# Kernel tuning notes

Hardware: AMD Instinct MI355X
Metric: run time of the kernel (lower is better)

Reference implementation:

```python
import jax, jax.numpy as jnp
import numpy as np
import math

H = 8
D_MODEL = 512
D_K = D_MODEL // H
DIM_G = 64
WAVE_LEN = 1000.0


def box_relational_embedding(f_g):
    # f_g: [B, N, 4] -> [B, N, N, 64] trigonometric geometry embedding
    x_min, y_min, x_max, y_max = jnp.split(f_g, 4, axis=-1)  # each [B,N,1]
    cx = (x_min + x_max) * 0.5
    cy = (y_min + y_max) * 0.5
    w = x_max - x_min + 1.0
    h = y_max - y_min + 1.0
    # pairwise deltas: [B,N,1] vs [B,1,N] -> [B,N,N]
    cx_t = jnp.swapaxes(cx, 1, 2)  # [B,1,N]
    cy_t = jnp.swapaxes(cy, 1, 2)
    w_t = jnp.swapaxes(w, 1, 2)
    h_t = jnp.swapaxes(h, 1, 2)
    delta_x = jnp.log(jnp.maximum(jnp.abs((cx - cx_t) / w), 0.001))
    delta_y = jnp.log(jnp.maximum(jnp.abs((cy - cy_t) / h), 0.001))
    delta_w = jnp.log(w / w_t)
    delta_h = jnp.log(h / h_t)
    position_mat = jnp.stack([delta_x, delta_y, delta_w, delta_h], axis=-1)  # [B,N,N,4]
    feat_range = jnp.arange(DIM_G // 8, dtype=position_mat.dtype) / (DIM_G / 8)
    dim_mat = 1.0 / jnp.power(jnp.asarray(WAVE_LEN, position_mat.dtype), feat_range)  # [8]
    mul_mat = (100.0 * position_mat)[..., None] * dim_mat  # [B,N,N,4,8]
    B, N = position_mat.shape[0], position_mat.shape[1]
    mul_mat = mul_mat.reshape(B, N, N, -1)  # [B,N,N,32]
    return jnp.concatenate([jnp.sin(mul_mat), jnp.cos(mul_mat)], axis=-1)  # [B,N,N,64]


def setup_inputs() -> dict:
    key = jax.random.key(0)
    ks = jax.random.split(key, 16)
    B, N = 16, 256
    scale = 1.0 / math.sqrt(D_MODEL)
    inp = {
        'input_query': jax.random.normal(ks[0], (B, N, D_MODEL), jnp.float32),
        'input_key': jax.random.normal(ks[1], (B, N, D_MODEL), jnp.float32),
        'input_value': jax.random.normal(ks[2], (B, N, D_MODEL), jnp.float32),
        'input_box': jax.random.uniform(ks[3], (B, N, 4), jnp.float32),
        'mask': jnp.ones((B, N), jnp.int32),
        # projection weights stored as [d_in, d_out] (x @ W + b)
        'Wq': jax.random.normal(ks[4], (D_MODEL, D_MODEL), jnp.float32) * scale,
        'bq': jnp.zeros((D_MODEL,), jnp.float32),
        'Wk': jax.random.normal(ks[5], (D_MODEL, D_MODEL), jnp.float32) * scale,
        'bk': jnp.zeros((D_MODEL,), jnp.float32),
        'Wv': jax.random.normal(ks[6], (D_MODEL, D_MODEL), jnp.float32) * scale,
        'bv': jnp.zeros((D_MODEL,), jnp.float32),
        'Wo': jax.random.normal(ks[7], (D_MODEL, D_MODEL), jnp.float32) * scale,
        'bo': jnp.zeros((D_MODEL,), jnp.float32),
        # 8 geometric-bias heads: Linear(64 -> 1) each, stacked -> [H, 64], [H]
        'WG_w': jax.random.normal(ks[8], (H, DIM_G), jnp.float32) * (1.0 / math.sqrt(DIM_G)),
        'WG_b': jnp.zeros((H,), jnp.float32),
    }
    return inp


def reference(input_query, input_key, input_value, input_box, mask,
              Wq, bq, Wk, bk, Wv, bv, Wo, bo, WG_w, WG_b):
    B, N, _ = input_query.shape

    def proj(x, W, b):  # [B,N,D] -> [B,H,N,d_k]
        return (x @ W + b).reshape(B, N, H, D_K).transpose(0, 2, 1, 3)

    q = proj(input_query, Wq, bq)
    k = proj(input_key, Wk, bk)
    v = proj(input_value, Wv, bv)

    geo = box_relational_embedding(input_box)  # [B,N,N,64]
    # per-head geometric weights, ReLU'd: [B,H,N,N]
    w_g = jax.nn.relu(jnp.einsum('bnmg,hg->bhnm', geo, WG_w) + WG_b[None, :, None, None])

    scaled_dot = jnp.einsum('bhqd,bhkd->bhqk', q, k) / np.sqrt(D_K).astype(q.dtype)
    # mask: [B,N] keys -> [B,1,1,N], broadcast over heads and queries
    scaled_dot = jnp.where(mask[:, None, None, :] == 0, jnp.asarray(-1e9, scaled_dot.dtype), scaled_dot)
    w_mn = jax.nn.softmax(jnp.log(jnp.maximum(w_g, 1e-6)) + scaled_dot, axis=-1)
    # dropout is identity in eval mode
    out = jnp.einsum('bhqk,bhkd->bhqd', w_mn, v)  # [B,H,N,d_k]
    out = out.transpose(0, 2, 1, 3).reshape(B, N, H * D_K)
    return out @ Wo + bo
```

## Files before the change

kernel.cpp:

```cpp
#include <hip/hip_runtime.h>
#include <hip/hip_fp16.h>
#include <math.h>

#define Bv   16
#define Nv   256
#define Dv   512
#define Hv   8
#define MNv  4096

typedef __attribute__((ext_vector_type(8))) short bf16x8;
typedef __attribute__((ext_vector_type(4))) float f32x4;
typedef __fp16 fp16x8 __attribute__((ext_vector_type(8)));
typedef __fp16 fp16x2 __attribute__((ext_vector_type(2)));

__device__ __forceinline__ unsigned short f2bf(float f) {
    unsigned u = __float_as_uint(f);
    u = u + 0x7FFFu + ((u >> 16) & 1u);
    return (unsigned short)(u >> 16);
}
__device__ __forceinline__ void gload_lds16(const void* g, void* l) {
    __builtin_amdgcn_global_load_lds(
        (const __attribute__((address_space(1))) unsigned int*)g,
        (__attribute__((address_space(3))) unsigned int*)l, 16, 0, 0);
}

__device__ __forceinline__ void fast_sincos(float x, float* s, float* c) {
    const float rev = x * 0.15915494309189535f;
    const float fr  = rev - floorf(rev);
    *s = __builtin_amdgcn_sinf(fr);
    *c = __builtin_amdgcn_cosf(fr);
}
__device__ __forceinline__ float fast_log(float x) {
    return __builtin_amdgcn_logf(x) * 0.6931471805599453f;
}
__device__ __forceinline__ float fast_exp(float x) {
    return __builtin_amdgcn_exp2f(x * 1.4426950408889634f);
}

__global__ __launch_bounds__(256) void mega1_kernel(
    const float* __restrict__ box, const int* __restrict__ mask,
    const float* __restrict__ WGw, const float* __restrict__ WGb,
    __half* __restrict__ LB,
    const float* __restrict__ xq, const float* __restrict__ xk,
    const float* __restrict__ xv, unsigned short* __restrict__ Ab,
    const float* __restrict__ Wq, const float* __restrict__ Wk,
    const float* __restrict__ Wv, const float* __restrict__ Wo,
    const float* __restrict__ bq, const float* __restrict__ bk,
    const float* __restrict__ bv, const float* __restrict__ bo,
    unsigned short* __restrict__ Wt, float* __restrict__ biasStack)
{
    __shared__ __align__(16) char smraw[64 * 65 * 4];
    const int bid = blockIdx.x;
    const int t = threadIdx.x;

    if (bid < 4096) {
        unsigned short (*Lst)[264] = (unsigned short (*)[264])smraw;
        const int q = bid & 255;
        const int b = bid >> 8;
        const int w = t >> 6, lane = t & 63;
        const int n = lane & 15;
        const int quad = lane >> 4;

        const float4 bq_ = *(const float4*)(box + (b * Nv + q) * 4);
        const float cxq = (bq_.x + bq_.z) * 0.5f;
        const float cyq = (bq_.y + bq_.w) * 0.5f;
        const float wq  = bq_.z - bq_.x + 1.0f;
        const float hq  = bq_.w - bq_.y + 1.0f;

        union F16x8 { fp16x8 v; fp16x2 p[4]; };
        F16x8 Bs_, Bc_;
        Bs_.v = (fp16x8){}; Bc_.v = (fp16x8){};
        float bias_n = 0.0f;
        if (n < Hv) {
            bias_n = WGb[n];
#pragma unroll
            for (int jj = 0; jj < 4; ++jj) {
                Bs_.p[jj] = __builtin_amdgcn_cvt_pkrtz(WGw[n * 64 + quad * 8 + 2 * jj],
                                                       WGw[n * 64 + quad * 8 + 2 * jj + 1]);
                Bc_.p[jj] = __builtin_amdgcn_cvt_pkrtz(WGw[n * 64 + 32 + quad * 8 + 2 * jj],
                                                       WGw[n * 64 + 32 + quad * 8 + 2 * jj + 1]);
            }
        }

        const float dimm[8] = {1.0f, 0.42169650342f, 0.17782794100f, 0.07498942093f,
                               0.03162277660f, 0.01333521432f, 0.00562341325f, 0.00237137371f};
        const bool isCtr = (quad < 2);
        const bool isY   = (quad & 1);
        const float cq  = isY ? cyq : cxq;
        const float sq_ = isY ? hq : wq;

#pragma unroll
        for (int i = 0; i < 4; ++i) {
            const int m0 = (w * 4 + i) * 16;
            const float4 bm = *(const float4*)(box + (b * Nv + m0 + n) * 4);
            const float cxm = (bm.x + bm.z) * 0.5f;
            const float cym = (bm.y + bm.w) * 0.5f;
            const float wm  = bm.z - bm.x + 1.0f;
            const float hm  = bm.w - bm.y + 1.0f;
            const float cm_ = isY ? cym : cxm;
            const float sm_ = isY ? hm : wm;
            const float top = isCtr ? fabsf(cq - cm_) : sq_;
            const float bot = isCtr ? sq_ : sm_;
            float r = top * __builtin_amdgcn_rcpf(bot);
            if (isCtr) r = fmaxf(r, 1e-3f);
            const float base = 69.31471805599453f * __builtin_amdgcn_logf(r);

            float sv[8], cv[8];
#pragma unroll
            for (int j = 0; j < 8; ++j)
                fast_sincos(base * dimm[j], &sv[j], &cv[j]);

            F16x8 As_, Ac_;
#pragma unroll
            for (int jj = 0; jj < 4; ++jj) {
                As_.p[jj] = __builtin_amdgcn_cvt_pkrtz(sv[2 * jj], sv[2 * jj + 1]);
                Ac_.p[jj] = __builtin_amdgcn_cvt_pkrtz(cv[2 * jj], cv[2 * jj + 1]);
            }

            f32x4 acc = {};
            acc = __builtin_amdgcn_mfma_f32_16x16x32_f16(As_.v, Bs_.v, acc, 0, 0, 0);
            acc = __builtin_amdgcn_mfma_f32_16x16x32_f16(Ac_.v, Bc_.v, acc, 0, 0, 0);

            const int mrow = m0 + quad * 4;
            const int4 mk = *(const int4*)(mask + b * Nv + mrow);
            if (n < Hv) {
                const int* mkp = (const int*)&mk;
                const int pos0 = quad * 64 + (w * 4 + i);
#pragma unroll
                for (int rr = 0; rr < 4; ++rr) {
                    const float val = fmaxf(acc[rr] + bias_n, 1e-6f);
                    const float lb = fast_log(val) + (mkp[rr] ? 0.0f : -30000.0f);
                    Lst[n][pos0 + rr * 16] = __half_as_ushort(__float2half(lb));
                }
            }
        }

        __syncthreads();
        const int h = t >> 5, c = t & 31;
        unsigned short* dst = (unsigned short*)LB +
                              ((size_t)(b * Hv + h) * Nv + q) * Nv + c * 8;
        *(int4*)dst = *(const int4*)&Lst[h][c * 8];

    } else if (bid < 10240) {
        const int i = bid - 4096;
        const int z = i >> 11;
        const int xblk = i & 2047;
        const float* src = (z == 0) ? xq : (z == 1) ? xk : xv;
        const size_t base = (size_t)z * (MNv * Dv);
        const int idx = (xblk * 256 + t) * 4;
        float4 x = *(const float4*)(src + idx);
        ushort4 h4;
        h4.x = f2bf(x.x); h4.y = f2bf(x.y); h4.z = f2bf(x.z); h4.w = f2bf(x.w);
        *(ushort4*)(Ab + base + idx) = h4;

    } else {
        float (*T)[65] = (float (*)[65])smraw;
        const int i = bid - 10240;
        const int z = i >> 6;
        const int rem = i & 63;
        const int n0 = (rem & 7) * 64, k0 = (rem >> 3) * 64;
        const float* W = (z == 0) ? Wq : (z == 1) ? Wk : (z == 2) ? Wv : Wo;
        const float* b = (z == 0) ? bq : (z == 1) ? bk : (z == 2) ? bv : bo;
        const int col = t & 63, rb = t >> 6;
#pragma unroll
        for (int j = 0; j < 16; ++j) {
            const int row = j * 4 + rb;
            T[row][col] = W[(k0 + row) * Dv + n0 + col];
        }
        __syncthreads();
#pragma unroll
        for (int j = 0; j < 16; ++j) {
            const int row = j * 4 + rb;
            Wt[z * (Dv * Dv) + (n0 + row) * Dv + k0 + col] = f2bf(T[col][row]);
        }
        if (rem == 0) {
            biasStack[z * Dv + t]       = b[t];
            biasStack[z * Dv + t + 256] = b[t + 256];
        }
    }
}

__global__ __launch_bounds__(256) void qkv_gemm_kernel(
    const unsigned short* __restrict__ Ab, const unsigned short* __restrict__ Wt,
    const float* __restrict__ bst, unsigned short* __restrict__ Qb2,
    unsigned short* __restrict__ Kb2, unsigned short* __restrict__ Vt2)
{
    const int z = blockIdx.z;
    const unsigned short* A = Ab + (size_t)z * (MNv * Dv);
    const unsigned short* Wz = Wt + (size_t)z * (Dv * Dv);
    const float* bias = bst + z * Dv;

    const int n0 = blockIdx.x * 64;
    const int m0 = blockIdx.y * 128;
    const int t = threadIdx.x;
    const int w = t >> 6, lane = t & 63;
    const int wm = w & 1, wn = w >> 1;

    __shared__ unsigned short As[128][32];
    __shared__ unsigned short Bs[64][32];

    f32x4 acc[4][2] = {};

    const int sr = lane >> 2;
    const int sk = (lane & 3) * 8;
    const int fr = lane & 15;
    const int fk = (lane >> 4) * 8;

    for (int k0 = 0; k0 < Dv; k0 += 32) {
        __syncthreads();
#pragma unroll
        for (int j = 0; j < 2; ++j) {
            const int row = w * 32 + j * 16 + sr;
            gload_lds16(A + (size_t)(m0 + row) * Dv + k0 + sk, &As[w * 32 + j * 16][0]);
        }
        gload_lds16(Wz + (size_t)(n0 + w * 16 + sr) * Dv + k0 + sk, &Bs[w * 16][0]);
        __syncthreads();

        bf16x8 af[4], bfr[2];
#pragma unroll
        for (int mt = 0; mt < 4; ++mt)
            af[mt] = *(const bf16x8*)&As[wm * 64 + mt * 16 + fr][fk];
#pragma unroll
        for (int nt = 0; nt < 2; ++nt)
            bfr[nt] = *(const bf16x8*)&Bs[wn * 32 + nt * 16 + fr][fk];
#pragma unroll
        for (int mt = 0; mt < 4; ++mt)
#pragma unroll
            for (int nt = 0; nt < 2; ++nt)
                acc[mt][nt] = __builtin_amdgcn_mfma_f32_16x16x32_bf16(
                    af[mt], bfr[nt], acc[mt][nt], 0, 0, 0);
    }

    const int er = (lane >> 4) * 4;
    const int ec = lane & 15;
    const float scale = (z == 0) ? 0.125f : 1.0f;
#pragma unroll
    for (int nt = 0; nt < 2; ++nt) {
        const int gn = n0 + wn * 32 + nt * 16 + ec;
        const float bv_ = bias[gn];
#pragma unroll
        for (int mt = 0; mt < 4; ++mt) {
            const int gm = m0 + wm * 64 + mt * 16 + er;
            if (z == 2) {
                ushort4 o;
                o.x = f2bf(acc[mt][nt][0] + bv_);
                o.y = f2bf(acc[mt][nt][1] + bv_);
                o.z = f2bf(acc[mt][nt][2] + bv_);
                o.w = f2bf(acc[mt][nt][3] + bv_);
                *(ushort4*)(Vt2 + ((size_t)(gm >> 8) * Dv + gn) * Nv + (gm & 255)) = o;
            } else {
                unsigned short* cp = ((z == 0) ? Qb2 : Kb2) + (size_t)gm * Dv + gn;
#pragma unroll
                for (int r = 0; r < 4; ++r)
                    cp[(size_t)r * Dv] = f2bf((acc[mt][nt][r] + bv_) * scale);
            }
        }
    }
}

__global__ __launch_bounds__(256) void out_gemm_kernel(
    const unsigned short* __restrict__ A, const unsigned short* __restrict__ Wz,
    const float* __restrict__ bias, float* __restrict__ C)
{
    const int n0 = blockIdx.x * 64;
    const int m0 = blockIdx.y * 128;
    const int t = threadIdx.x;
    const int w = t >> 6, lane = t & 63;
    const int wm = w & 1, wn = w >> 1;

    __shared__ unsigned short As[128][32];
    __shared__ unsigned short Bs[64][32];

    f32x4 acc[4][2] = {};

    const int sr = lane >> 2;
    const int sk = (lane & 3) * 8;
    const int fr = lane & 15;
    const int fk = (lane >> 4) * 8;

    for (int k0 = 0; k0 < Dv; k0 += 32) {
        __syncthreads();
#pragma unroll
        for (int j = 0; j < 2; ++j) {
            const int row = w * 32 + j * 16 + sr;
            gload_lds16(A + (size_t)(m0 + row) * Dv + k0 + sk, &As[w * 32 + j * 16][0]);
        }
        gload_lds16(Wz + (size_t)(n0 + w * 16 + sr) * Dv + k0 + sk, &Bs[w * 16][0]);
        __syncthreads();

        bf16x8 af[4], bfr[2];
#pragma unroll
        for (int mt = 0; mt < 4; ++mt)
            af[mt] = *(const bf16x8*)&As[wm * 64 + mt * 16 + fr][fk];
#pragma unroll
        for (int nt = 0; nt < 2; ++nt)
            bfr[nt] = *(const bf16x8*)&Bs[wn * 32 + nt * 16 + fr][fk];
#pragma unroll
        for (int mt = 0; mt < 4; ++mt)
#pragma unroll
            for (int nt = 0; nt < 2; ++nt)
                acc[mt][nt] = __builtin_amdgcn_mfma_f32_16x16x32_bf16(
                    af[mt], bfr[nt], acc[mt][nt], 0, 0, 0);
    }

    const int er = (lane >> 4) * 4;
    const int ec = lane & 15;
#pragma unroll
    for (int nt = 0; nt < 2; ++nt) {
        const int gn = n0 + wn * 32 + nt * 16 + ec;
        const float bv_ = bias[gn];
#pragma unroll
        for (int mt = 0; mt < 4; ++mt) {
            const int gm = m0 + wm * 64 + mt * 16 + er;
            float* cp = C + (size_t)gm * Dv + gn;
#pragma unroll
            for (int r = 0; r < 4; ++r)
                cp[(size_t)r * Dv] = acc[mt][nt][r] + bv_;
        }
    }
}

__global__ __launch_bounds__(256) void attn3_kernel(
    const unsigned short* __restrict__ Qb2, const unsigned short* __restrict__ Kb2,
    const unsigned short* __restrict__ Vt2, const __half* __restrict__ LB,
    unsigned short* __restrict__ CTXb)
{
    const int qt = blockIdx.x, h = blockIdx.y, b = blockIdx.z;
    const int q0 = qt * 64;
    const int t = threadIdx.x, w = t >> 6, lane = t & 63;
    const int fr = lane & 15, fq = lane >> 4;

    __shared__ unsigned short Qs[64][72];
    __shared__ unsigned short Ks[256][72];
    __shared__ unsigned short Vt[64][264];
    unsigned short (*Pb)[264] = (unsigned short (*)[264])&Ks[0][0];

#pragma unroll
    for (int i = 0; i < 2; ++i) {
        const int idx = t + i * 256;
        const int row = idx >> 3, cu = idx & 7;
        *(bf16x8*)&Qs[row][cu * 8] =
            *(const bf16x8*)(Qb2 + (size_t)(b * Nv + q0 + row) * Dv + h * 64 + cu * 8);
    }
#pragma unroll
    for (int i = 0; i < 8; ++i) {
        const int idx = t + i * 256;
        const int row = idx >> 3, cu = idx & 7;
        *(bf16x8*)&Ks[row][cu * 8] =
            *(const bf16x8*)(Kb2 + (size_t)(b * Nv + row) * Dv + h * 64 + cu * 8);
    }
#pragma unroll
    for (int i = 0; i < 8; ++i) {
        const int idx = t + i * 256;
        const int row = idx >> 5, cu = idx & 31;
        *(bf16x8*)&Vt[row][cu * 8] =
            *(const bf16x8*)(Vt2 + (size_t)b * (Dv * Nv) + (h * 64 + row) * Nv + cu * 8);
    }

    f32x4 acc[16];
    const int qb = q0 + w * 16 + fq * 4;
    const __half* lbp = LB + ((size_t)(b * Hv + h) * Nv + qb) * Nv + fr * 16;
#pragma unroll
    for (int r = 0; r < 4; ++r) {
        union { int4 v; __half hs[8]; } u0, u1;
        const int4* p = (const int4*)(lbp + (size_t)r * Nv);
        u0.v = p[0]; u1.v = p[1];
#pragma unroll
        for (int nt = 0; nt < 8; ++nt) acc[nt][r]     = __half2float(u0.hs[nt]);
#pragma unroll
        for (int nt = 0; nt < 8; ++nt) acc[nt + 8][r] = __half2float(u1.hs[nt]);
    }

    __syncthreads();

    const bf16x8 aq0 = *(const bf16x8*)&Qs[w * 16 + fr][fq * 8];
    const bf16x8 aq1 = *(const bf16x8*)&Qs[w * 16 + fr][32 + fq * 8];
#pragma unroll
    for (int nt = 0; nt < 16; ++nt) {
        const bf16x8 bk0 = *(const bf16x8*)&Ks[nt * 16 + fr][fq * 8];
        const bf16x8 bk1 = *(const bf16x8*)&Ks[nt * 16 + fr][32 + fq * 8];
        acc[nt] = __builtin_amdgcn_mfma_f32_16x16x32_bf16(aq0, bk0, acc[nt], 0, 0, 0);
        acc[nt] = __builtin_amdgcn_mfma_f32_16x16x32_bf16(aq1, bk1, acc[nt], 0, 0, 0);
    }

    float ri[4];
#pragma unroll
    for (int r = 0; r < 4; ++r) {
        float mx = acc[0][r];
#pragma unroll
        for (int nt = 1; nt < 16; ++nt) mx = fmaxf(mx, acc[nt][r]);
        mx = fmaxf(mx, __shfl_xor(mx, 1));
        mx = fmaxf(mx, __shfl_xor(mx, 2));
        mx = fmaxf(mx, __shfl_xor(mx, 4));
        mx = fmaxf(mx, __shfl_xor(mx, 8));
        float s = 0.0f;
#pragma unroll
        for (int nt = 0; nt < 16; ++nt) {
            const float e = fast_exp(acc[nt][r] - mx);
            acc[nt][r] = e;
            s += e;
        }
        s += __shfl_xor(s, 1);
        s += __shfl_xor(s, 2);
        s += __shfl_xor(s, 4);
        s += __shfl_xor(s, 8);
        ri[r] = __builtin_amdgcn_rcpf(s);
    }

    __syncthreads();

#pragma unroll
    for (int nt = 0; nt < 16; ++nt)
#pragma unroll
        for (int r = 0; r < 4; ++r)
            Pb[w * 16 + fq * 4 + r][nt * 16 + fr] = f2bf(acc[nt][r] * ri[r]);

    f32x4 o[4] = {};
#pragma unroll
    for (int kt = 0; kt < 8; ++kt) {
        const bf16x8 ap = *(const bf16x8*)&Pb[w * 16 + fr][kt * 32 + fq * 8];
#pragma unroll
        for (int nt2 = 0; nt2 < 4; ++nt2) {
            const bf16x8 bv_ = *(const bf16x8*)&Vt[nt2 * 16 + fr][kt * 32 + fq * 8];
            o[nt2] = __builtin_amdgcn_mfma_f32_16x16x32_bf16(ap, bv_, o[nt2], 0, 0, 0);
        }
    }

#pragma unroll
    for (int nt2 = 0; nt2 < 4; ++nt2)
#pragma unroll
        for (int r = 0; r < 4; ++r)
            CTXb[(size_t)(b * Nv + qb + r) * Dv + h * 64 + nt2 * 16 + fr] =
                f2bf(o[nt2][r]);
}

extern "C" void kernel_launch(void* const* d_in, const int* in_sizes, int n_in,
                              void* d_out, int out_size, void* d_ws, size_t ws_size,
                              hipStream_t stream) {
    (void)in_sizes; (void)n_in; (void)out_size; (void)ws_size;

    const float* inq  = (const float*)d_in[0];
    const float* ink  = (const float*)d_in[1];
    const float* inv  = (const float*)d_in[2];
    const float* box  = (const float*)d_in[3];
    const int*   mask = (const int*)d_in[4];
    const float* Wq   = (const float*)d_in[5];
    const float* bq   = (const float*)d_in[6];
    const float* Wk   = (const float*)d_in[7];
    const float* bk   = (const float*)d_in[8];
    const float* Wv   = (const float*)d_in[9];
    const float* bv   = (const float*)d_in[10];
    const float* Wo   = (const float*)d_in[11];
    const float* bo   = (const float*)d_in[12];
    const float* WGw  = (const float*)d_in[13];
    const float* WGb  = (const float*)d_in[14];

    char* W = (char*)d_ws;
    const size_t MB = 1048576;
    unsigned short* Qb2  = (unsigned short*)(W + 0);
    unsigned short* Kb2  = (unsigned short*)(W + 4 * MB);
    unsigned short* Vt2  = (unsigned short*)(W + 8 * MB);
    unsigned short* Wt   = (unsigned short*)(W + 12 * MB);
    float*          bst  = (float*)(W + 14 * MB);
    unsigned short* CTXb = (unsigned short*)(W + 15 * MB);
    unsigned short* Ab   = (unsigned short*)(W + 20 * MB);
    __half*         LB   = (__half*)(W + 32 * MB);

    float* out = (float*)d_out;

    mega1_kernel<<<10496, 256, 0, stream>>>(
        box, mask, WGw, WGb, LB,
        inq, ink, inv, Ab,
        Wq, Wk, Wv, Wo, bq, bk, bv, bo, Wt, bst);

    qkv_gemm_kernel<<<dim3(8, 32, 3), 256, 0, stream>>>(Ab, Wt, bst, Qb2, Kb2, Vt2);

    attn3_kernel<<<dim3(4, 8, 16), 256, 0, stream>>>(Qb2, Kb2, Vt2, LB, CTXb);

    out_gemm_kernel<<<dim3(8, 32), 256, 0, stream>>>(CTXb, Wt + 3 * (Dv * Dv), bst + 3 * Dv, out);
}
```

Baseline: 156.6 us.

## Double-buffer GEMM K-loop and use direct global-to-LDS loads in attention

The QKV and output projection GEMMs now stage K-tiles of 64 into a double-buffered LDS layout. The next tile is prefetched with global_load_lds while MFMAs run on the current one, and there is one barrier per iteration instead of two. The attention kernel loads Q, K and V^T straight into LDS through global_load_lds using split 32-wide layouts instead of register round-trips, and it issues the log-bias loads first so they overlap with these. LDS use per block grows, which may reduce occupancy, and the unpadded 32-column layouts may cause bank conflicts.

```diff
diff --git a/kernel.cpp b/kernel.cpp
--- a/kernel.cpp
+++ b/kernel.cpp
@@ -196,39 +196,56 @@
     const int w = t >> 6, lane = t & 63;
     const int wm = w & 1, wn = w >> 1;
 
-    __shared__ unsigned short As[128][32];
-    __shared__ unsigned short Bs[64][32];
+    __shared__ __align__(16) unsigned short As[2][2][128][32];
+    __shared__ __align__(16) unsigned short Bs[2][2][64][32];
 
     f32x4 acc[4][2] = {};
 
-    const int sr = lane >> 2;
-    const int sk = (lane & 3) * 8;
+    const int sr = t >> 2;
+    const int sc = (t & 3) * 8;
     const int fr = lane & 15;
-    const int fk = (lane >> 4) * 8;
-
-    for (int k0 = 0; k0 < Dv; k0 += 32) {
+    const int fq = lane >> 4;
+
+    auto STAGE = [&](int bu, int k0) {
+#pragma unroll
+        for (int kk = 0; kk < 2; ++kk) {
+#pragma unroll
+            for (int i = 0; i < 2; ++i)
+                gload_lds16(A + (size_t)(m0 + i * 64 + sr) * Dv + k0 + kk * 32 + sc,
+                            &As[bu][kk][i * 64 + w * 16][0]);
+            gload_lds16(Wz + (size_t)(n0 + sr) * Dv + k0 + kk * 32 + sc,
+                        &Bs[bu][kk][w * 16][0]);
+        }
+    };
+
+    STAGE(0, 0);
+    __syncthreads();
+    int cur = 0;
+#pragma unroll
+    for (int kt = 0; kt < 8; ++kt) {
+        if (kt < 7) STAGE(cur ^ 1, (kt + 1) * 64);
+
+        bf16x8 af[2][4], bfr[2][2];
+#pragma unroll
+        for (int kk = 0; kk < 2; ++kk) {
+#pragma unroll
+            for (int mt = 0; mt < 4; ++mt)
+                af[kk][mt] = *(const bf16x8*)&As[cur][kk][wm * 64 + mt * 16 + fr][fq * 8];
+#pragma unroll
+            for (int nt = 0; nt < 2; ++nt)
+                bfr[kk][nt] = *(const bf16x8*)&Bs[cur][kk][wn * 32 + nt * 16 + fr][fq * 8];
+        }
+#pragma unroll
+        for (int mt = 0; mt < 4; ++mt)
+#pragma unroll
+            for (int nt = 0; nt < 2; ++nt) {
+                acc[mt][nt] = __builtin_amdgcn_mfma_f32_16x16x32_bf16(
+                    af[0][mt], bfr[0][nt], acc[mt][nt], 0, 0, 0);
+                acc[mt][nt] = __builtin_amdgcn_mfma_f32_16x16x32_bf16(
+                    af[1][mt], bfr[1][nt], acc[mt][nt], 0, 0, 0);
+            }
         __syncthreads();
-#pragma unroll
-        for (int j = 0; j < 2; ++j) {
-            const int row = w * 32 + j * 16 + sr;
-            gload_lds16(A + (size_t)(m0 + row) * Dv + k0 + sk, &As[w * 32 + j * 16][0]);
-        }
-        gload_lds16(Wz + (size_t)(n0 + w * 16 + sr) * Dv + k0 + sk, &Bs[w * 16][0]);
-        __syncthreads();
-
-        bf16x8 af[4], bfr[2];
-#pragma unroll
-        for (int mt = 0; mt < 4; ++mt)
-            af[mt] = *(const bf16x8*)&As[wm * 64 + mt * 16 + fr][fk];
-#pragma unroll
-        for (int nt = 0; nt < 2; ++nt)
-            bfr[nt] = *(const bf16x8*)&Bs[wn * 32 + nt * 16 + fr][fk];
-#pragma unroll
-        for (int mt = 0; mt < 4; ++mt)
-#pragma unroll
-            for (int nt = 0; nt < 2; ++nt)
-                acc[mt][nt] = __builtin_amdgcn_mfma_f32_16x16x32_bf16(
-                    af[mt], bfr[nt], acc[mt][nt], 0, 0, 0);
+        cur ^= 1;
     }
 
     const int er = (lane >> 4) * 4;
@@ -268,39 +285,56 @@
     const int w = t >> 6, lane = t & 63;
     const int wm = w & 1, wn = w >> 1;
 
-    __shared__ unsigned short As[128][32];
-    __shared__ unsigned short Bs[64][32];
+    __shared__ __align__(16) unsigned short As[2][2][128][32];
+    __shared__ __align__(16) unsigned short Bs[2][2][64][32];
 
     f32x4 acc[4][2] = {};
 
-    const int sr = lane >> 2;
-    const int sk = (lane & 3) * 8;
+    const int sr = t >> 2;
+    const int sc = (t & 3) * 8;
     const int fr = lane & 15;
-    const int fk = (lane >> 4) * 8;
-
-    for (int k0 = 0; k0 < Dv; k0 += 32) {
+    const int fq = lane >> 4;
+
+    auto STAGE = [&](int bu, int k0) {
+#pragma unroll
+        for (int kk = 0; kk < 2; ++kk) {
+#pragma unroll
+            for (int i = 0; i < 2; ++i)
+                gload_lds16(A + (size_t)(m0 + i * 64 + sr) * Dv + k0 + kk * 32 + sc,
+                            &As[bu][kk][i * 64 + w * 16][0]);
+            gload_lds16(Wz + (size_t)(n0 + sr) * Dv + k0 + kk * 32 + sc,
+                        &Bs[bu][kk][w * 16][0]);
+        }
+    };
+
+    STAGE(0, 0);
+    __syncthreads();
+    int cur = 0;
+#pragma unroll
+    for (int kt = 0; kt < 8; ++kt) {
+        if (kt < 7) STAGE(cur ^ 1, (kt + 1) * 64);
+
+        bf16x8 af[2][4], bfr[2][2];
+#pragma unroll
+        for (int kk = 0; kk < 2; ++kk) {
+#pragma unroll
+            for (int mt = 0; mt < 4; ++mt)
+                af[kk][mt] = *(const bf16x8*)&As[cur][kk][wm * 64 + mt * 16 + fr][fq * 8];
+#pragma unroll
+            for (int nt = 0; nt < 2; ++nt)
+                bfr[kk][nt] = *(const bf16x8*)&Bs[cur][kk][wn * 32 + nt * 16 + fr][fq * 8];
+        }
+#pragma unroll
+        for (int mt = 0; mt < 4; ++mt)
+#pragma unroll
+            for (int nt = 0; nt < 2; ++nt) {
+                acc[mt][nt] = __builtin_amdgcn_mfma_f32_16x16x32_bf16(
+                    af[0][mt], bfr[0][nt], acc[mt][nt], 0, 0, 0);
+                acc[mt][nt] = __builtin_amdgcn_mfma_f32_16x16x32_bf16(
+                    af[1][mt], bfr[1][nt], acc[mt][nt], 0, 0, 0);
+            }
         __syncthreads();
-#pragma unroll
-        for (int j = 0; j < 2; ++j) {
-            const int row = w * 32 + j * 16 + sr;
-            gload_lds16(A + (size_t)(m0 + row) * Dv + k0 + sk, &As[w * 32 + j * 16][0]);
-        }
-        gload_lds16(Wz + (size_t)(n0 + w * 16 + sr) * Dv + k0 + sk, &Bs[w * 16][0]);
-        __syncthreads();
-
-        bf16x8 af[4], bfr[2];
-#pragma unroll
-        for (int mt = 0; mt < 4; ++mt)
-            af[mt] = *(const bf16x8*)&As[wm * 64 + mt * 16 + fr][fk];
-#pragma unroll
-        for (int nt = 0; nt < 2; ++nt)
-            bfr[nt] = *(const bf16x8*)&Bs[wn * 32 + nt * 16 + fr][fk];
-#pragma unroll
-        for (int mt = 0; mt < 4; ++mt)
-#pragma unroll
-            for (int nt = 0; nt < 2; ++nt)
-                acc[mt][nt] = __builtin_amdgcn_mfma_f32_16x16x32_bf16(
-                    af[mt], bfr[nt], acc[mt][nt], 0, 0, 0);
+        cur ^= 1;
     }
 
     const int er = (lane >> 4) * 4;
@@ -330,55 +364,62 @@
     const int t = threadIdx.x, w = t >> 6, lane = t & 63;
     const int fr = lane & 15, fq = lane >> 4;
 
-    __shared__ unsigned short Qs[64][72];
-    __shared__ unsigned short Ks[256][72];
-    __shared__ unsigned short Vt[64][264];
-    unsigned short (*Pb)[264] = (unsigned short (*)[264])&Ks[0][0];
-
-#pragma unroll
-    for (int i = 0; i < 2; ++i) {
-        const int idx = t + i * 256;
-        const int row = idx >> 3, cu = idx & 7;
-        *(bf16x8*)&Qs[row][cu * 8] =
-            *(const bf16x8*)(Qb2 + (size_t)(b * Nv + q0 + row) * Dv + h * 64 + cu * 8);
-    }
-#pragma unroll
-    for (int i = 0; i < 8; ++i) {
-        const int idx = t + i * 256;
-        const int row = idx >> 3, cu = idx & 7;
-        *(bf16x8*)&Ks[row][cu * 8] =
-            *(const bf16x8*)(Kb2 + (size_t)(b * Nv + row) * Dv + h * 64 + cu * 8);
-    }
-#pragma unroll
-    for (int i = 0; i < 8; ++i) {
-        const int idx = t + i * 256;
-        const int row = idx >> 5, cu = idx & 31;
-        *(bf16x8*)&Vt[row][cu * 8] =
-            *(const bf16x8*)(Vt2 + (size_t)b * (Dv * Nv) + (h * 64 + row) * Nv + cu * 8);
-    }
-
-    f32x4 acc[16];
+    __shared__ __align__(16) unsigned short smem[36864];
+    unsigned short (*K0)[32] = (unsigned short (*)[32])&smem[0];
+    unsigned short (*K1)[32] = (unsigned short (*)[32])&smem[8192];
+    unsigned short (*Q0)[32] = (unsigned short (*)[32])&smem[16384];
+    unsigned short (*Q1)[32] = (unsigned short (*)[32])&smem[18432];
+    unsigned short (*Vs)[32] = (unsigned short (*)[32])&smem[20480];
+    unsigned short (*Pb)[264] = (unsigned short (*)[264])&smem[0];
+
+    const int sr = t >> 2;
+    const int sc = (t & 3) * 8;
+
     const int qb = q0 + w * 16 + fq * 4;
     const __half* lbp = LB + ((size_t)(b * Hv + h) * Nv + qb) * Nv + fr * 16;
+    int4 lbv[4][2];
 #pragma unroll
     for (int r = 0; r < 4; ++r) {
-        union { int4 v; __half hs[8]; } u0, u1;
         const int4* p = (const int4*)(lbp + (size_t)r * Nv);
-        u0.v = p[0]; u1.v = p[1];
-#pragma unroll
-        for (int nt = 0; nt < 8; ++nt) acc[nt][r]     = __half2float(u0.hs[nt]);
-#pragma unroll
-        for (int nt = 0; nt < 8; ++nt) acc[nt + 8][r] = __half2float(u1.hs[nt]);
+        lbv[r][0] = p[0];
+        lbv[r][1] = p[1];
+    }
+
+#pragma unroll
+    for (int i = 0; i < 4; ++i) {
+        gload_lds16(Kb2 + (size_t)(b * Nv + i * 64 + sr) * Dv + h * 64 + sc,
+                    &K0[i * 64 + w * 16][0]);
+        gload_lds16(Kb2 + (size_t)(b * Nv + i * 64 + sr) * Dv + h * 64 + 32 + sc,
+                    &K1[i * 64 + w * 16][0]);
+    }
+    gload_lds16(Qb2 + (size_t)(b * Nv + q0 + sr) * Dv + h * 64 + sc,
+                &Q0[w * 16][0]);
+    gload_lds16(Qb2 + (size_t)(b * Nv + q0 + sr) * Dv + h * 64 + 32 + sc,
+                &Q1[w * 16][0]);
+#pragma unroll
+    for (int kt = 0; kt < 8; ++kt)
+        gload_lds16(Vt2 + (size_t)b * (Dv * Nv) + (h * 64 + sr) * Nv + kt * 32 + sc,
+                    &Vs[kt * 64 + w * 16][0]);
+
+    f32x4 acc[16];
+#pragma unroll
+    for (int r = 0; r < 4; ++r) {
+        const __half* hs0 = (const __half*)&lbv[r][0];
+        const __half* hs1 = (const __half*)&lbv[r][1];
+#pragma unroll
+        for (int nt = 0; nt < 8; ++nt) acc[nt][r]     = __half2float(hs0[nt]);
+#pragma unroll
+        for (int nt = 0; nt < 8; ++nt) acc[nt + 8][r] = __half2float(hs1[nt]);
     }
 
     __syncthreads();
 
-    const bf16x8 aq0 = *(const bf16x8*)&Qs[w * 16 + fr][fq * 8];
-    const bf16x8 aq1 = *(const bf16x8*)&Qs[w * 16 + fr][32 + fq * 8];
+    const bf16x8 aq0 = *(const bf16x8*)&Q0[w * 16 + fr][fq * 8];
+    const bf16x8 aq1 = *(const bf16x8*)&Q1[w * 16 + fr][fq * 8];
 #pragma unroll
     for (int nt = 0; nt < 16; ++nt) {
-        const bf16x8 bk0 = *(const bf16x8*)&Ks[nt * 16 + fr][fq * 8];
-        const bf16x8 bk1 = *(const bf16x8*)&Ks[nt * 16 + fr][32 + fq * 8];
+        const bf16x8 bk0 = *(const bf16x8*)&K0[nt * 16 + fr][fq * 8];
+        const bf16x8 bk1 = *(const bf16x8*)&K1[nt * 16 + fr][fq * 8];
         acc[nt] = __builtin_amdgcn_mfma_f32_16x16x32_bf16(aq0, bk0, acc[nt], 0, 0, 0);
         acc[nt] = __builtin_amdgcn_mfma_f32_16x16x32_bf16(aq1, bk1, acc[nt], 0, 0, 0);
     }
@@ -421,7 +462,7 @@
         const bf16x8 ap = *(const bf16x8*)&Pb[w * 16 + fr][kt * 32 + fq * 8];
 #pragma unroll
         for (int nt2 = 0; nt2 < 4; ++nt2) {
-            const bf16x8 bv_ = *(const bf16x8*)&Vt[nt2 * 16 + fr][kt * 32 + fq * 8];
+            const bf16x8 bv_ = *(const bf16x8*)&Vs[kt * 64 + nt2 * 16 + fr][fq * 8];
             o[nt2] = __builtin_amdgcn_mfma_f32_16x16x32_bf16(ap, bv_, o[nt2], 0, 0, 0);
         }
     }
```

Measured after the change: 157.0 us. About the same (+0.3%).
